# Kernel tuning notes

Hardware: AMD Instinct MI355X
Metric: run time of the kernel (lower is better)

The kernel has to match this reference:

```python
import jax, jax.numpy as jnp
import numpy as np

N = 8192          # num_people
H = 128           # hidden_dim
ZE = 64           # zone_embed_dim
TE = 32           # temporal_embed_dim
NZ = 100          # num_zones
GRU_IN = H + ZE + TE


def _lin(k, out_d, in_d):
    kw, kb = jax.random.split(k)
    bound = 1.0 / np.sqrt(in_d)
    W = jax.random.uniform(kw, (out_d, in_d), minval=-bound, maxval=bound, dtype=jnp.float32)
    b = jax.random.uniform(kb, (out_d,), minval=-bound, maxval=bound, dtype=jnp.float32)
    return W, b


def setup_inputs() -> dict:
    key = jax.random.key(0)
    ks = jax.random.split(key, 12)
    t = jax.random.uniform(ks[0], (1,), dtype=jnp.float32)
    person_h = jax.random.normal(ks[1], (N, H), dtype=jnp.float32)
    gnn_zone_embeds = jax.random.normal(ks[2], (NZ, ZE), dtype=jnp.float32)
    W_time, b_time = _lin(ks[3], TE, 1)
    W_loc, b_loc = _lin(ks[4], NZ, H)
    Wq, bq = _lin(ks[5], H, H)
    Wk, bk = _lin(ks[6], H, H)
    Wv, bv = _lin(ks[7], H, H)
    W_merge, b_merge = _lin(ks[8], H, 2 * H)
    W_ih, b_ih = _lin(ks[9], 3 * H, GRU_IN)
    W_hh, b_hh = _lin(ks[10], 3 * H, H)
    ln_gamma = jnp.ones((H,), jnp.float32)
    ln_beta = jnp.zeros((H,), jnp.float32)
    return dict(t=t, person_h=person_h, gnn_zone_embeds=gnn_zone_embeds,
                W_time=W_time, b_time=b_time, W_loc=W_loc, b_loc=b_loc,
                Wq=Wq, bq=bq, Wk=Wk, bk=bk, Wv=Wv, bv=bv,
                W_merge=W_merge, b_merge=b_merge,
                W_ih=W_ih, b_ih=b_ih, W_hh=W_hh, b_hh=b_hh,
                ln_gamma=ln_gamma, ln_beta=ln_beta)


def reference(t, person_h, gnn_zone_embeds, W_time, b_time, W_loc, b_loc,
              Wq, bq, Wk, bk, Wv, bv, W_merge, b_merge,
              W_ih, b_ih, W_hh, b_hh, ln_gamma, ln_beta):
    n = person_h.shape[0]
    # spatial context: soft location distribution over zones
    loc_probs = jax.nn.softmax(person_h @ W_loc.T + b_loc, axis=-1)   # [N, NZ]
    spatial_context = loc_probs @ gnn_zone_embeds                     # [N, ZE]
    # leave-one-out social attention == full attention with diagonal masked
    q = person_h @ Wq.T + bq                                          # [N, H]
    k = person_h @ Wk.T + bk
    v = person_h @ Wv.T + bv
    scores = (q @ k.T) / np.sqrt(H).astype(np.float32)                # [N, N]
    diag = jnp.eye(n, dtype=bool)
    scores = jnp.where(diag, -jnp.inf, scores)
    attn = jax.nn.softmax(scores, axis=-1)
    social_context = attn @ v                                         # [N, H]
    h_interacted = jnp.concatenate([person_h, social_context], axis=-1) @ W_merge.T + b_merge
    time_context = jnp.broadcast_to(t.reshape(1, 1), (n, 1)) @ W_time.T + b_time  # [N, TE]
    gru_input = jnp.concatenate([h_interacted, spatial_context, time_context], axis=-1)
    # torch.nn.GRUCell: gates order (reset, update, new)
    gx = gru_input @ W_ih.T + b_ih                                    # [N, 3H]
    gh = person_h @ W_hh.T + b_hh
    xr, xz, xn = jnp.split(gx, 3, axis=-1)
    hr, hz, hn = jnp.split(gh, 3, axis=-1)
    r = jax.nn.sigmoid(xr + hr)
    z = jax.nn.sigmoid(xz + hz)
    ng = jnp.tanh(xn + r * hn)
    h_new = (1.0 - z) * ng + z * person_h
    d = h_new - person_h
    mu = jnp.mean(d, axis=-1, keepdims=True)
    var = jnp.var(d, axis=-1, keepdims=True)
    d = (d - mu) * jax.lax.rsqrt(var + 1e-5) * ln_gamma + ln_beta
    return d
```

## Files before the change

kernel.cpp:

```cpp
#include <hip/hip_runtime.h>


typedef __attribute__((ext_vector_type(8)))  short bf16x8;
typedef __attribute__((ext_vector_type(4)))  float f32x4;
typedef __attribute__((ext_vector_type(16))) float f32x16;
typedef __attribute__((ext_vector_type(4)))  unsigned uint4v;

#define N_P   8192
#define H_D   128
#define NCHNK 8
#define CHLEN (N_P / NCHNK)
#define KVB   64
#define NTIL  (CHLEN / KVB)
#define LDE   384

#if __has_builtin(__builtin_amdgcn_exp2f)
#define EXP2(x) __builtin_amdgcn_exp2f(x)
#else
#define EXP2(x) exp2f(x)
#endif

__device__ __forceinline__ short f2bf(float f) {
  unsigned u = __float_as_uint(f);
  u = (u + 0x7fffu + ((u >> 16) & 1u)) >> 16;
  return (short)u;
}
__device__ __forceinline__ float bf2f(short s) {
  return __uint_as_float(((unsigned)(unsigned short)s) << 16);
}

__device__ __forceinline__ int swzb(int row, int slot, int nslots) {
  return (row * nslots + (slot ^ (row & ((nslots - 1) & 7)))) << 4;
}

__device__ __forceinline__ unsigned cvtpk(float a, float b) {
  unsigned d;
  asm("v_cvt_pk_bf16_f32 %0, %1, %2" : "=v"(d) : "v"(a), "v"(b));
  return d;
}

__device__ __forceinline__ void swap32(unsigned& a, unsigned& b) {
#if __has_builtin(__builtin_amdgcn_permlane32_swap)
  auto r = __builtin_amdgcn_permlane32_swap(a, b, false, false);
  a = r[0]; b = r[1];
#else
  asm volatile("v_permlane32_swap_b32 %0, %1" : "+v"(a), "+v"(b));
#endif
}

typedef __attribute__((address_space(1))) const void GV;
typedef __attribute__((address_space(3))) void LV;
__device__ __forceinline__ void gld_lds16(const void* g, void* l) {
  __builtin_amdgcn_global_load_lds((GV*)g, (LV*)l, 16, 0, 0);
}

__constant__ const float QSCALE = 0.12751551485988857f;
#define LOG2E 1.4426950408889634f

__global__ __launch_bounds__(256) void init_kernel(
    const float* t, const float* W_time, const float* b_time,
    const float* W_loc, const float* b_loc,
    const float* Wq, const float* bq, const float* Wk, const float* bk,
    const float* Wv, const float* bv,
    const float* W_merge, const float* b_merge,
    const float* W_ih, const float* b_ih,
    const float* W_hh, const float* b_hh,
    const float* ph,
    short* W1, float* bias1, short* W_big, float* bias_big, short* PH2e) {
  const int b = blockIdx.x, tidl = threadIdx.x;
  if (b < 64) {
    int tid = b * 256 + tidl, stride = 64 * 256;
    for (int i = tid; i < 512 * 128; i += stride) {
      int r = i >> 7, k = i & 127;
      float v;
      if (r < 128)      v = Wq[r * 128 + k];
      else if (r < 256) v = Wk[(r - 128) * 128 + k];
      else if (r < 384) v = Wv[(r - 256) * 128 + k];
      else if (r < 484) v = W_loc[(r - 384) * 128 + k];
      else              v = 0.f;
      W1[i] = f2bf(v);
    }
    for (int i = tid; i < 512; i += stride) {
      float v;
      if (i < 128)      v = bq[i];
      else if (i < 256) v = bk[i - 128];
      else if (i < 384) v = bv[i - 256];
      else if (i < 484) v = b_loc[i - 384];
      else              v = 0.f;
      bias1[i] = v;
    }
  } else if (b < 576) {
    __shared__ float rowj[128];
    const int n = b - 64;
    if (tidl < 128) rowj[tidl] = (n < 384) ? W_ih[n * 224 + tidl] : 0.f;
    __syncthreads();
    {
      float acc = 0.f;
      if (n < 384) {
#pragma unroll 8
        for (int j = 0; j < 128; ++j) acc += rowj[j] * W_merge[j * 256 + tidl];
      }
      if (tidl < 128) {
        if (n < 256)      acc += W_hh[n * 128 + tidl];
        else if (n >= 384) acc = W_hh[(n - 128) * 128 + tidl];
      }
      W_big[n * 384 + tidl] = f2bf(acc);
    }
    if (tidl < 128) {
      int k2 = 256 + tidl;
      float v = 0.f;
      if (n < 384) {
        if (k2 < 320)      v = W_ih[n * 224 + 128 + (k2 - 256)];
        else if (k2 < 352) v = W_ih[n * 224 + 192 + (k2 - 320)];
      }
      W_big[n * 384 + k2] = f2bf(v);
    }
    if (tidl < 64) {
      float p = rowj[tidl] * b_merge[tidl] + rowj[tidl + 64] * b_merge[tidl + 64];
#pragma unroll
      for (int mk = 1; mk < 64; mk <<= 1) p += __shfl_xor(p, mk);
      if (tidl == 0) {
        float bb;
        if (n < 256)      bb = b_ih[n] + p + b_hh[n];
        else if (n < 384) bb = b_ih[n] + p;
        else              bb = b_hh[n - 128];
        bias_big[n] = bb;
      }
    }
  } else {
    int tid = (b - 576) * 256 + tidl, stride = 1024 * 256;
    for (int i = tid; i < N_P * H_D; i += stride) {
      int r = i >> 7, d = i & 127;
      PH2e[r * LDE + d] = f2bf(ph[i]);
    }
    const float t0 = t[0];
    for (int i = tid; i < N_P * 64; i += stride) {
      int r = i >> 6, j = i & 63;
      float v = (j < 32) ? (t0 * W_time[j] + b_time[j]) : 0.f;
      PH2e[r * LDE + 320 + j] = f2bf(v);
    }
  }
}

template <int MODE, int K>
__global__ __launch_bounds__(256, 3) void gemm64_kernel(
    const short* __restrict__ X, int ldx, const short* __restrict__ W,
    const float* __restrict__ bias,
    short* out_q, short* out_k, short* out_vT, float* out_loc,
    short* out_gx) {
  __shared__ short Xl[64 * 128];
  __shared__ short Wl[128 * 128];
  const int tid = threadIdx.x;
  const int bm = blockIdx.x * 64, bn = blockIdx.y * 128;
  const int l = tid & 63, wid = tid >> 6;
  const int g = l >> 4, c = l & 15;
  const int wr = wid >> 1, wc = wid & 1;
  f32x4 acc[2][4] = {};
  constexpr int KT = K / 128;
#pragma unroll 1
  for (int kt = 0; kt < KT; ++kt) {
    const int k0 = kt * 128;
#pragma unroll
    for (int pass = 0; pass < 4; ++pass) {
      int s = tid + pass * 256;
      int row = s >> 4, p = s & 15;
      int lsl = p ^ (row & 7);
      gld_lds16(X + (size_t)(bm + row) * ldx + k0 + lsl * 8, (char*)Xl + s * 16);
    }
#pragma unroll
    for (int pass = 0; pass < 8; ++pass) {
      int s = tid + pass * 256;
      int row = s >> 4, p = s & 15;
      int lsl = p ^ (row & 7);
      gld_lds16(W + (size_t)(bn + row) * K + k0 + lsl * 8, (char*)Wl + s * 16);
    }
    __syncthreads();
#pragma unroll
    for (int kc = 0; kc < 4; ++kc) {
      bf16x8 a[2], bfr[4];
#pragma unroll
      for (int mi = 0; mi < 2; ++mi)
        a[mi] = *(const bf16x8*)((const char*)Xl + swzb(wr * 32 + mi * 16 + c, kc * 4 + g, 16));
#pragma unroll
      for (int ni = 0; ni < 4; ++ni)
        bfr[ni] = *(const bf16x8*)((const char*)Wl + swzb(wc * 64 + ni * 16 + c, kc * 4 + g, 16));
#pragma unroll
      for (int mi = 0; mi < 2; ++mi)
#pragma unroll
        for (int ni = 0; ni < 4; ++ni)
          acc[mi][ni] = __builtin_amdgcn_mfma_f32_16x16x32_bf16(a[mi], bfr[ni], acc[mi][ni], 0, 0, 0);
    }
    if (kt + 1 < KT) __syncthreads();
  }
  if constexpr (MODE == 0) {
    if (blockIdx.y == 2) {
      __syncthreads();
      short* T = Wl;
#pragma unroll
      for (int mi = 0; mi < 2; ++mi)
#pragma unroll
        for (int ni = 0; ni < 4; ++ni)
#pragma unroll
          for (int r = 0; r < 4; ++r) {
            int rl = wr * 32 + mi * 16 + 4 * g + r;
            int cl = wc * 64 + ni * 16 + c;
            T[rl * 130 + cl] = f2bf(acc[mi][ni][r] + bias[256 + cl]);
          }
      __syncthreads();
#pragma unroll
      for (int pass = 0; pass < 32; ++pass) {
        int d = pass * 4 + (tid >> 6);
        int j = tid & 63;
        out_vT[(size_t)d * N_P + bm + j] = T[j * 130 + d];
      }
    } else {
#pragma unroll
      for (int mi = 0; mi < 2; ++mi)
#pragma unroll
        for (int ni = 0; ni < 4; ++ni)
#pragma unroll
          for (int r = 0; r < 4; ++r) {
            int row = bm + wr * 32 + mi * 16 + 4 * g + r;
            int col = bn + wc * 64 + ni * 16 + c;
            float val = acc[mi][ni][r] + bias[col];
            if (col < 128)      out_q[row * 128 + col] = f2bf(val * QSCALE);
            else if (col < 256) out_k[row * 128 + col - 128] = f2bf(val);
            else if (col >= 384 && col < 484) out_loc[row * 112 + col - 384] = val;
          }
    }
  } else {
#pragma unroll
    for (int mi = 0; mi < 2; ++mi)
#pragma unroll
      for (int ni = 0; ni < 4; ++ni)
#pragma unroll
        for (int r = 0; r < 4; ++r) {
          int row = bm + wr * 32 + mi * 16 + 4 * g + r;
          int col = bn + wc * 64 + ni * 16 + c;
          out_gx[row * 512 + col] = f2bf(acc[mi][ni][r] + bias[col]);
        }
  }
}

__global__ __launch_bounds__(256, 2) void attn_kernel(
    const short* __restrict__ qb, const short* __restrict__ kb,
    const short* __restrict__ vT, short* __restrict__ pacc,
    float* __restrict__ pml) {
  __shared__ short Kl[2][KVB * H_D];
  __shared__ short Vl[2][H_D * KVB];
  const int tid = threadIdx.x;
  const int qbk = blockIdx.x >> 3, ch = blockIdx.x & 7;
  const int chbase = ch * CHLEN;
  const int l = tid & 63, wid = tid >> 6;
  const int c32 = l & 31, hi = l >> 5;
  const int qrow0w = qbk * 128 + wid * 32;

  char* ldsK = (char*)&Kl[0][0];
  char* ldsV = (char*)&Vl[0][0];

  auto stage = [&](int b, int tt) {
    const int off = tt * KVB;
#pragma unroll
    for (int j = 0; j < 4; ++j) {
      const int i = tid + j * 256;
      const int kr = i >> 4, ks = (i & 15) ^ (kr & 15);
      gld_lds16(kb + (size_t)(chbase + off + kr) * 128 + ks * 8,
                ldsK + b * 16384 + i * 16);
      const int vr = i >> 3, vs = (i & 7) ^ (vr & 7);
      gld_lds16(vT + (size_t)vr * N_P + chbase + off + vs * 8,
                ldsV + b * 16384 + i * 16);
    }
  };

  bf16x8 qf[8];
#pragma unroll
  for (int sl = 0; sl < 8; ++sl)
    qf[sl] = *(const bf16x8*)(qb + (size_t)(qrow0w + c32) * 128 + sl * 16 + hi * 8);

  bf16x8 ones;
#pragma unroll
  for (int j = 0; j < 8; ++j) ones[j] = (short)0x3F80;

  const int c15 = c32 & 15;
  const int kbase0 = c32 * 256;
  int koff[8];
#pragma unroll
  for (int sl = 0; sl < 8; ++sl) koff[sl] = ((2 * sl + hi) ^ c15) << 4;
  const int xh = (c32 >> 1) & 3, x0 = c32 & 1;
  const int xb = (hi ^ x0) << 4;
  int voff[4], vbase[4];
#pragma unroll
  for (int s4 = 0; s4 < 4; ++s4) voff[s4] = (s4 ^ xh) << 5;
#pragma unroll
  for (int db = 0; db < 4; ++db) vbase[db] = (db * 32 + c32) * 128 + xb;

  f32x16 acc[4] = {};
  f32x16 accl = {};
  float m = -1e30f;

  stage(0, 0);
  asm volatile("s_waitcnt vmcnt(0)" ::: "memory");
  __builtin_amdgcn_s_barrier();
  int cur = 0;

#pragma unroll 1
  for (int t = 0; t < NTIL; ++t) {
    if (t + 1 < NTIL) stage(cur ^ 1, t + 1);

    const int kv0 = chbase + t * KVB;
    const char* Kb = (const char*)&Kl[cur][0];
    const char* Vb = (const char*)&Vl[cur][0];

    f32x16 s0 = {}, s1 = {};
    __builtin_amdgcn_s_setprio(1);
#pragma unroll
    for (int sl = 0; sl < 8; ++sl) {
      bf16x8 k0 = *(const bf16x8*)(Kb + kbase0 + koff[sl]);
      bf16x8 k1 = *(const bf16x8*)(Kb + kbase0 + 8192 + koff[sl]);
      s0 = __builtin_amdgcn_mfma_f32_32x32x16_bf16(k0, qf[sl], s0, 0, 0, 0);
      s1 = __builtin_amdgcn_mfma_f32_32x32x16_bf16(k1, qf[sl], s1, 0, 0, 0);
    }
    __builtin_amdgcn_s_setprio(0);

    if (qrow0w + 32 > kv0 && qrow0w < kv0 + 64) {
      const int qr = qrow0w + c32;
#pragma unroll
      for (int r = 0; r < 16; ++r) {
        const int rowp = (r & 3) + 8 * (r >> 2) + 4 * hi;
        s0[r] = (kv0 + rowp == qr) ? -1e30f : s0[r];
        s1[r] = (kv0 + 32 + rowp == qr) ? -1e30f : s1[r];
      }
    }

    if (t == 0) {
      f32x16 mx;
#pragma unroll
      for (int r = 0; r < 16; ++r) mx[r] = fmaxf(s0[r], s1[r]);
#pragma unroll
      for (int w2 = 8; w2 >= 1; w2 >>= 1)
#pragma unroll
        for (int r = 0; r < w2; ++r) mx[r] = fmaxf(mx[r], mx[r + w2]);
      m = fmaxf(mx[0], __shfl_xor(mx[0], 32));
    }

#pragma unroll
    for (int r = 0; r < 16; ++r) s0[r] = EXP2(s0[r] - m);
#pragma unroll
    for (int r = 0; r < 16; ++r) s1[r] = EXP2(s1[r] - m);

    auto pvslice = [&](const f32x16& ss, int base, int sl4) {
      unsigned dA = cvtpk(ss[base + 0], ss[base + 1]);
      unsigned dB = cvtpk(ss[base + 2], ss[base + 3]);
      unsigned dC = cvtpk(ss[base + 4], ss[base + 5]);
      unsigned dD = cvtpk(ss[base + 6], ss[base + 7]);
      swap32(dA, dC);
      swap32(dB, dD);
      uint4v w = {dA, dB, dC, dD};
      bf16x8 pa = __builtin_bit_cast(bf16x8, w);
#pragma unroll
      for (int db = 0; db < 4; ++db) {
        bf16x8 vfr = *(const bf16x8*)(Vb + vbase[db] + voff[sl4]);
        acc[db] = __builtin_amdgcn_mfma_f32_32x32x16_bf16(pa, vfr, acc[db], 0, 0, 0);
      }
      accl = __builtin_amdgcn_mfma_f32_32x32x16_bf16(pa, ones, accl, 0, 0, 0);
    };
    __builtin_amdgcn_s_setprio(1);
    pvslice(s0, 0, 0);
    pvslice(s0, 8, 1);
    pvslice(s1, 0, 2);
    pvslice(s1, 8, 3);
    __builtin_amdgcn_s_setprio(0);

    if (t + 1 < NTIL) {
      asm volatile("s_waitcnt vmcnt(0)" ::: "memory");
      __builtin_amdgcn_s_barrier();
      asm volatile("" ::: "memory");
    }
    cur ^= 1;
  }

#pragma unroll
  for (int db = 0; db < 4; ++db)
#pragma unroll
    for (int r = 0; r < 16; ++r) {
      const int qr = qrow0w + (r & 3) + 8 * (r >> 2) + 4 * hi;
      pacc[((size_t)ch * N_P + qr) * 128 + db * 32 + c32] = f2bf(acc[db][r]);
    }
  {
    const int rr = (c32 & 3) | (((c32 >> 3) & 3) << 2);
    float own = (((c32 >> 2) & 1) == hi) ? accl[rr] : 0.f;
    float lv = own + __shfl_xor(own, 32);
    if (hi == 0) {
      const int qr = qrow0w + c32;
      pml[((size_t)ch * N_P + qr) * 2]     = m;
      pml[((size_t)ch * N_P + qr) * 2 + 1] = lv;
    }
  }
}

__global__ __launch_bounds__(256) void combine_spatial_kernel(
    const short* __restrict__ pacc, const float* __restrict__ pml,
    const float* __restrict__ locf, const float* __restrict__ E,
    short* __restrict__ PH2e) {
  const int b = blockIdx.x, tid = threadIdx.x;
  if (b < 4096) {
    int row = b * 2 + (tid >> 7);
    int d = tid & 127;
    float mv[NCHNK], lv[NCHNK], M = -1e30f;
#pragma unroll
    for (int cc = 0; cc < NCHNK; ++cc) {
      mv[cc] = pml[(cc * N_P + row) * 2];
      lv[cc] = pml[(cc * N_P + row) * 2 + 1];
      M = fmaxf(M, mv[cc]);
    }
    float L = 0.f, O = 0.f;
#pragma unroll
    for (int cc = 0; cc < NCHNK; ++cc) {
      float w = EXP2(mv[cc] - M);
      L += lv[cc] * w;
      O += bf2f(pacc[((size_t)cc * N_P + row) * 128 + d]) * w;
    }
    PH2e[row * LDE + 128 + d] = f2bf(O / L);
  } else {
    __shared__ float pl[4][104];
    int wid = tid >> 6, l = tid & 63;
    int row = (b - 4096) * 4 + wid;
    float v0 = locf[row * 112 + l];
    float v1 = (l + 64 < 100) ? locf[row * 112 + 64 + l] : -1e30f;
    float m = fmaxf(v0, v1);
#pragma unroll
    for (int mk = 1; mk < 64; mk <<= 1) m = fmaxf(m, __shfl_xor(m, mk));
    float p0 = EXP2((v0 - m) * LOG2E);
    float p1 = (l + 64 < 100) ? EXP2((v1 - m) * LOG2E) : 0.f;
    float s = p0 + p1;
#pragma unroll
    for (int mk = 1; mk < 64; mk <<= 1) s += __shfl_xor(s, mk);
    float inv = 1.f / s;
    pl[wid][l] = p0 * inv;
    if (l + 64 < 100) pl[wid][64 + l] = p1 * inv;
    float acc = 0.f;
#pragma unroll 4
    for (int z = 0; z < 100; ++z) acc += pl[wid][z] * E[z * 64 + l];
    PH2e[row * LDE + 256 + l] = f2bf(acc);
  }
}

__global__ __launch_bounds__(256) void final_kernel(const short* __restrict__ gxs,
                                                    const float* __restrict__ ph,
                                                    const float* __restrict__ gamma,
                                                    const float* __restrict__ beta,
                                                    float* __restrict__ out) {
  int tid = threadIdx.x, wid = tid >> 6, l = tid & 63;
  int row = blockIdx.x * 4 + wid;
  float dd[2];
#pragma unroll
  for (int half = 0; half < 2; ++half) {
    int d = l + 64 * half;
    float h  = ph[row * 128 + d];
    float sr = bf2f(gxs[row * 512 + d]);
    float sz = bf2f(gxs[row * 512 + 128 + d]);
    float xn = bf2f(gxs[row * 512 + 256 + d]);
    float hn = bf2f(gxs[row * 512 + 384 + d]);
    float r = 1.f / (1.f + EXP2(-LOG2E * sr));
    float z = 1.f / (1.f + EXP2(-LOG2E * sz));
    float a = xn + r * hn;
    float ng = 1.f - 2.f / (1.f + EXP2(2.f * LOG2E * a));
    dd[half] = (1.f - z) * (ng - h);
  }
  float s = dd[0] + dd[1], ss = dd[0] * dd[0] + dd[1] * dd[1];
#pragma unroll
  for (int mk = 1; mk < 64; mk <<= 1) {
    s += __shfl_xor(s, mk);
    ss += __shfl_xor(ss, mk);
  }
  float mu = s * (1.f / 128.f);
  float var = ss * (1.f / 128.f) - mu * mu;
  float rs = rsqrtf(var + 1e-5f);
#pragma unroll
  for (int half = 0; half < 2; ++half) {
    int d = l + 64 * half;
    out[row * 128 + d] = (dd[half] - mu) * rs * gamma[d] + beta[d];
  }
}

extern "C" void kernel_launch(void* const* d_in, const int* in_sizes, int n_in,
                              void* d_out, int out_size, void* d_ws, size_t ws_size,
                              hipStream_t stream) {
  const float* t       = (const float*)d_in[0];
  const float* ph      = (const float*)d_in[1];
  const float* E       = (const float*)d_in[2];
  const float* W_time  = (const float*)d_in[3];
  const float* b_time  = (const float*)d_in[4];
  const float* W_loc   = (const float*)d_in[5];
  const float* b_loc   = (const float*)d_in[6];
  const float* Wq      = (const float*)d_in[7];
  const float* bq      = (const float*)d_in[8];
  const float* Wk      = (const float*)d_in[9];
  const float* bk      = (const float*)d_in[10];
  const float* Wv      = (const float*)d_in[11];
  const float* bv      = (const float*)d_in[12];
  const float* W_merge = (const float*)d_in[13];
  const float* b_merge = (const float*)d_in[14];
  const float* W_ih    = (const float*)d_in[15];
  const float* b_ih    = (const float*)d_in[16];
  const float* W_hh    = (const float*)d_in[17];
  const float* b_hh    = (const float*)d_in[18];
  const float* gamma   = (const float*)d_in[19];
  const float* beta    = (const float*)d_in[20];
  float* out = (float*)d_out;

  char* w = (char*)d_ws;
  auto alloc = [&](size_t bytes) {
    char* p = w;
    w += (bytes + 255) & ~(size_t)255;
    return p;
  };
  short* W1      = (short*)alloc(512 * 128 * 2);
  float* bias1   = (float*)alloc(512 * 4);
  short* W_big   = (short*)alloc(512 * 384 * 2);
  float* bias_big= (float*)alloc(512 * 4);
  short* PH2e    = (short*)alloc((size_t)N_P * LDE * 2);
  short* qbuf    = (short*)alloc((size_t)N_P * 128 * 2);
  short* kbuf    = (short*)alloc((size_t)N_P * 128 * 2);
  short* vT      = (short*)alloc((size_t)128 * N_P * 2);
  float* locf    = (float*)alloc((size_t)N_P * 112 * 4);
  short* gxs     = (short*)alloc((size_t)N_P * 512 * 2);
  short* pacc    = (short*)alloc((size_t)NCHNK * N_P * 128 * 2);
  float* pml     = (float*)alloc((size_t)NCHNK * N_P * 2 * 4);

  init_kernel<<<1600, 256, 0, stream>>>(t, W_time, b_time, W_loc, b_loc, Wq, bq,
                                        Wk, bk, Wv, bv, W_merge, b_merge,
                                        W_ih, b_ih, W_hh, b_hh, ph,
                                        W1, bias1, W_big, bias_big, PH2e);
  gemm64_kernel<0, 128><<<dim3(128, 4), 256, 0, stream>>>(
      PH2e, LDE, W1, bias1, qbuf, kbuf, vT, locf, nullptr);
  attn_kernel<<<512, 256, 0, stream>>>(qbuf, kbuf, vT, pacc, pml);
  combine_spatial_kernel<<<6144, 256, 0, stream>>>(pacc, pml, locf, E, PH2e);
  gemm64_kernel<2, 384><<<dim3(128, 4), 256, 0, stream>>>(
      PH2e, LDE, W_big, bias_big, nullptr, nullptr, nullptr, nullptr, gxs);
  final_kernel<<<2048, 256, 0, stream>>>(gxs, ph, gamma, beta, out);
}
```

Measured before the change: 88.43 us.

## Split attention KV into 12 uneven chunks with single-buffered V and scalar row-sum

Result: slower. 97.55 us (+10.3%).

```diff
diff --git a/kernel.cpp b/kernel.cpp
--- a/kernel.cpp
+++ b/kernel.cpp
@@ -8,10 +8,8 @@
 
 #define N_P   8192
 #define H_D   128
-#define NCHNK 8
-#define CHLEN (N_P / NCHNK)
+#define NCHNK 12
 #define KVB   64
-#define NTIL  (CHLEN / KVB)
 #define LDE   384
 
 #if __has_builtin(__builtin_amdgcn_exp2f)
@@ -242,33 +240,42 @@
   }
 }
 
-__global__ __launch_bounds__(256, 2) void attn_kernel(
+__global__ __launch_bounds__(256, 3) void attn_kernel(
     const short* __restrict__ qb, const short* __restrict__ kb,
     const short* __restrict__ vT, short* __restrict__ pacc,
     float* __restrict__ pml) {
   __shared__ short Kl[2][KVB * H_D];
-  __shared__ short Vl[2][H_D * KVB];
+  __shared__ short Vl[H_D * KVB];
   const int tid = threadIdx.x;
-  const int qbk = blockIdx.x >> 3, ch = blockIdx.x & 7;
-  const int chbase = ch * CHLEN;
+  const int qbk = blockIdx.x / 12, ch = blockIdx.x % 12;
+  const int tile0 = ch * 10 + (ch < 8 ? ch : 8);
+  const int nt = (ch < 8) ? 11 : 10;
+  const int chbase = tile0 * KVB;
   const int l = tid & 63, wid = tid >> 6;
   const int c32 = l & 31, hi = l >> 5;
   const int qrow0w = qbk * 128 + wid * 32;
 
   char* ldsK = (char*)&Kl[0][0];
-  char* ldsV = (char*)&Vl[0][0];
-
-  auto stage = [&](int b, int tt) {
-    const int off = tt * KVB;
+  char* ldsV = (char*)&Vl[0];
+
+  auto stageK = [&](int b, int tt) {
+    const int off = (tile0 + tt) * KVB;
 #pragma unroll
     for (int j = 0; j < 4; ++j) {
       const int i = tid + j * 256;
       const int kr = i >> 4, ks = (i & 15) ^ (kr & 15);
-      gld_lds16(kb + (size_t)(chbase + off + kr) * 128 + ks * 8,
+      gld_lds16(kb + (size_t)(off + kr) * 128 + ks * 8,
                 ldsK + b * 16384 + i * 16);
+    }
+  };
+  auto stageV = [&](int tt) {
+    const int off = (tile0 + tt) * KVB;
+#pragma unroll
+    for (int j = 0; j < 4; ++j) {
+      const int i = tid + j * 256;
       const int vr = i >> 3, vs = (i & 7) ^ (vr & 7);
-      gld_lds16(vT + (size_t)vr * N_P + chbase + off + vs * 8,
-                ldsV + b * 16384 + i * 16);
+      gld_lds16(vT + (size_t)vr * N_P + off + vs * 8,
+                ldsV + i * 16);
     }
   };
 
@@ -276,10 +283,6 @@
 #pragma unroll
   for (int sl = 0; sl < 8; ++sl)
     qf[sl] = *(const bf16x8*)(qb + (size_t)(qrow0w + c32) * 128 + sl * 16 + hi * 8);
-
-  bf16x8 ones;
-#pragma unroll
-  for (int j = 0; j < 8; ++j) ones[j] = (short)0x3F80;
 
   const int c15 = c32 & 15;
   const int kbase0 = c32 * 256;
@@ -295,21 +298,24 @@
   for (int db = 0; db < 4; ++db) vbase[db] = (db * 32 + c32) * 128 + xb;
 
   f32x16 acc[4] = {};
-  f32x16 accl = {};
-  float m = -1e30f;
-
-  stage(0, 0);
+  float m = -1e30f, lsum = 0.f;
+
+  stageK(0, 0);
+  stageV(0);
+  stageK(1, 1);
   asm volatile("s_waitcnt vmcnt(0)" ::: "memory");
   __builtin_amdgcn_s_barrier();
-  int cur = 0;
 
 #pragma unroll 1
-  for (int t = 0; t < NTIL; ++t) {
-    if (t + 1 < NTIL) stage(cur ^ 1, t + 1);
+  for (int t = 0; t < nt; ++t) {
+    const int cur = t & 1;
+    if (t + 1 < nt) { asm volatile("s_waitcnt vmcnt(8)" ::: "memory"); }
+    else            { asm volatile("s_waitcnt vmcnt(4)" ::: "memory"); }
+    __builtin_amdgcn_s_barrier();
+    asm volatile("" ::: "memory");
 
     const int kv0 = chbase + t * KVB;
-    const char* Kb = (const char*)&Kl[cur][0];
-    const char* Vb = (const char*)&Vl[cur][0];
+    const char* Kb = ldsK + cur * 16384;
 
     f32x16 s0 = {}, s1 = {};
     __builtin_amdgcn_s_setprio(1);
@@ -347,6 +353,11 @@
     for (int r = 0; r < 16; ++r) s0[r] = EXP2(s0[r] - m);
 #pragma unroll
     for (int r = 0; r < 16; ++r) s1[r] = EXP2(s1[r] - m);
+
+    if (t + 1 < nt) { asm volatile("s_waitcnt vmcnt(4)" ::: "memory"); }
+    else            { asm volatile("s_waitcnt vmcnt(0)" ::: "memory"); }
+    __builtin_amdgcn_s_barrier();
+    asm volatile("" ::: "memory");
 
     auto pvslice = [&](const f32x16& ss, int base, int sl4) {
       unsigned dA = cvtpk(ss[base + 0], ss[base + 1]);
@@ -359,10 +370,11 @@
       bf16x8 pa = __builtin_bit_cast(bf16x8, w);
 #pragma unroll
       for (int db = 0; db < 4; ++db) {
-        bf16x8 vfr = *(const bf16x8*)(Vb + vbase[db] + voff[sl4]);
+        bf16x8 vfr = *(const bf16x8*)(ldsV + vbase[db] + voff[sl4]);
         acc[db] = __builtin_amdgcn_mfma_f32_32x32x16_bf16(pa, vfr, acc[db], 0, 0, 0);
       }
-      accl = __builtin_amdgcn_mfma_f32_32x32x16_bf16(pa, ones, accl, 0, 0, 0);
+#pragma unroll
+      for (int j = 0; j < 8; ++j) lsum += ss[base + j];
     };
     __builtin_amdgcn_s_setprio(1);
     pvslice(s0, 0, 0);
@@ -371,12 +383,12 @@
     pvslice(s1, 8, 3);
     __builtin_amdgcn_s_setprio(0);
 
-    if (t + 1 < NTIL) {
-      asm volatile("s_waitcnt vmcnt(0)" ::: "memory");
+    if (t + 1 < nt) {
       __builtin_amdgcn_s_barrier();
       asm volatile("" ::: "memory");
-    }
-    cur ^= 1;
+      stageV(t + 1);
+      if (t + 2 < nt) stageK(cur, t + 2);
+    }
   }
 
 #pragma unroll
@@ -387,9 +399,7 @@
       pacc[((size_t)ch * N_P + qr) * 128 + db * 32 + c32] = f2bf(acc[db][r]);
     }
   {
-    const int rr = (c32 & 3) | (((c32 >> 3) & 3) << 2);
-    float own = (((c32 >> 2) & 1) == hi) ? accl[rr] : 0.f;
-    float lv = own + __shfl_xor(own, 32);
+    float lv = lsum + __shfl_xor(lsum, 32);
     if (hi == 0) {
       const int qr = qrow0w + c32;
       pml[((size_t)ch * N_P + qr) * 2]     = m;
@@ -534,7 +544,7 @@
                                         W1, bias1, W_big, bias_big, PH2e);
   gemm64_kernel<0, 128><<<dim3(128, 4), 256, 0, stream>>>(
       PH2e, LDE, W1, bias1, qbuf, kbuf, vT, locf, nullptr);
-  attn_kernel<<<512, 256, 0, stream>>>(qbuf, kbuf, vT, pacc, pml);
+  attn_kernel<<<768, 256, 0, stream>>>(qbuf, kbuf, vT, pacc, pml);
   combine_spatial_kernel<<<6144, 256, 0, stream>>>(pacc, pml, locf, E, PH2e);
   gemm64_kernel<2, 384><<<dim3(128, 4), 256, 0, stream>>>(
       PH2e, LDE, W_big, bias_big, nullptr, nullptr, nullptr, nullptr, gxs);
```
